# Optimization experiments

Measured on AMD Instinct MI355X. Metric: run time of the kernel, lower is better.

Reference implementation:

```python
import jax, jax.numpy as jnp
import numpy as np

TAU = 10.0 / 7.0
V_TH = 1.0
ALPHA = 10.0  # sigmoid surrogate slope

@jax.custom_vjp
def spike_fn(v):
    # Heaviside(v - v_th) forward, sigmoid surrogate backward
    return (v >= V_TH).astype(v.dtype)

def _spike_fwd(v):
    return spike_fn(v), v

def _spike_bwd(v, g):
    s = jax.nn.sigmoid(ALPHA * (v - V_TH))
    return (g * ALPHA * s * (1.0 - s),)

spike_fn.defvjp(_spike_fwd, _spike_bwd)

def lif_multistep(x_bctm):
    # x: [B, C, T, M]; LIF recurrence over T axis, v_reset=0 hard reset,
    # decay_input=True: v = v + (x - v)/tau
    x_t = jnp.moveaxis(x_bctm, 2, 0)  # [T, B, C, M]
    def step(v, x):
        v = v + (x - v) / TAU
        s = spike_fn(v)
        v = v * (1.0 - s)  # hard reset to 0 (not detached)
        return v, s
    v0 = jnp.zeros_like(x_t[0])
    _, s_t = jax.lax.scan(step, v0, x_t)
    return jnp.moveaxis(s_t, 0, 2)  # [B, C, T, M]

def conv2d(x, w, pad, dil):
    return jax.lax.conv_general_dilated(
        x, w, window_strides=(1, 1),
        padding=[(pad[0], pad[0]), (pad[1], pad[1])],
        rhs_dilation=dil,
        dimension_numbers=('NCHW', 'OIHW', 'NCHW'))

def setup_inputs() -> dict:
    key = jax.random.key(0)
    k0, k1, k2, k3, k4 = jax.random.split(key, 5)
    B, T, M = 32, 128, 40
    x = jax.random.normal(k0, (B, 1, T, M), dtype=jnp.float32)
    # kaiming-ish init: std = 1/sqrt(fan_in)
    w1 = jax.random.normal(k1, (64, 1, 4, 3), dtype=jnp.float32) / np.sqrt(1 * 4 * 3)
    w2 = jax.random.normal(k2, (64, 64, 4, 3), dtype=jnp.float32) / np.sqrt(64 * 4 * 3)
    w3 = jax.random.normal(k3, (64, 64, 4, 3), dtype=jnp.float32) / np.sqrt(64 * 4 * 3)
    kw, kb = jax.random.split(k4)
    wf = jax.random.normal(kw, (12, 64 * 40), dtype=jnp.float32) / np.sqrt(64 * 40)
    bf = jnp.zeros((12,), dtype=jnp.float32)
    return {"x": x, "w1": w1, "w2": w2, "w3": w3, "wf": wf, "bf": bf}

def reference(x, w1, w2, w3, wf, bf):
    h = conv2d(x, w1, (2, 1), (1, 1))     # [B,64,T+1,40]
    h = lif_multistep(h)
    h = conv2d(h, w2, (6, 3), (4, 3))     # shape preserved
    h = lif_multistep(h)
    h = conv2d(h, w3, (24, 9), (16, 9))   # shape preserved
    h = lif_multistep(h)
    B, C, T, M = h.shape
    h = jnp.transpose(h, (0, 2, 1, 3)).reshape(B, T, C * M)  # flatten=True path
    y = h @ wf.T + bf                     # [B, T, 12]
    return y.mean(axis=1)                 # [B, 12]
```

## Files before the change

kernel.cpp:

```cpp
#include <hip/hip_runtime.h>


typedef __attribute__((ext_vector_type(8))) _Float16 v8h;
typedef __attribute__((ext_vector_type(16))) float v16f;
typedef _Float16 half_t;

#define NB 32
#define NC 64
#define NT 129
#define TIN 128
#define NM 40
#define MS8 80
#define ROWB8 3280
#define SROWB8 2560

__global__ void prep_wfrag(const float* __restrict__ w, uint4* __restrict__ wf) {
    int tid = blockIdx.x * 256 + threadIdx.x;
    if (tid >= 12288) return;
    int lane = tid & 63;
    int rest = tid >> 6;
    int hl = rest & 1;
    int ct = (rest >> 1) & 1;
    int cq = (rest >> 2) & 3;
    int tap = rest >> 4;
    int kh = tap / 3, kw = tap % 3;
    int co = ct * 32 + (lane & 31);
    unsigned short o[8];
#pragma unroll
    for (int jj = 0; jj < 8; jj++) {
        int ci = cq * 16 + (lane >> 5) * 8 + jj;
        float wv = w[((co * 64 + ci) * 4 + kh) * 3 + kw];
        _Float16 hi = (_Float16)wv;
        _Float16 val = hl ? (_Float16)((wv - (float)hi) * 2048.0f) : hi;
        unsigned short us;
        __builtin_memcpy(&us, &val, 2);
        o[jj] = us;
    }
    uint4 r;
    __builtin_memcpy(&r, o, 16);
    wf[tid] = r;
}

__global__ void conv1_lif1(const float* __restrict__ x, const float* __restrict__ w1,
                           unsigned char* __restrict__ s1) {
    const int mg = blockIdx.x;
    const int b = blockIdx.y;
    const int c = threadIdx.x & 63;
    const int ml = threadIdx.x >> 6;
    const int m = mg * 4 + ml;
    float w[4][3];
#pragma unroll
    for (int kh = 0; kh < 4; kh++)
#pragma unroll
        for (int kw = 0; kw < 3; kw++) w[kh][kw] = w1[(c * 4 + kh) * 3 + kw];
    const float* xb = x + (size_t)b * TIN * NM;

    float xw[12][3];
#pragma unroll
    for (int rr = 0; rr < 12; rr++)
#pragma unroll
        for (int kw = 0; kw < 3; kw++) xw[rr][kw] = 0.f;
#pragma unroll
    for (int rr = 2; rr < 4; rr++)
#pragma unroll
        for (int kw = 0; kw < 3; kw++) {
            int mc = m - 1 + kw;
            xw[rr][kw] = ((unsigned)mc < (unsigned)NM) ? xb[(rr - 2) * NM + mc] : 0.f;
        }

    unsigned char* orow = s1 + ((size_t)b * NT * NM + m) * 64 + c;
    float v = 0.f;
    const float TAUc = 10.0f / 7.0f;

    for (int tb = 0; tb < NT; tb += 8) {
#pragma unroll
        for (int q = 0; q < 8; q++) {
            int row = tb + 2 + q;
#pragma unroll
            for (int kw = 0; kw < 3; kw++) {
                int mc = m - 1 + kw;
                xw[4 + q][kw] = (row < TIN && (unsigned)mc < (unsigned)NM)
                                    ? xb[row * NM + mc] : 0.f;
            }
        }
        int kmax = (NT - tb) < 8 ? (NT - tb) : 8;
#pragma unroll
        for (int k = 0; k < 8; k++) {
            if (k < kmax) {
                float uacc = 0.f;
#pragma unroll
                for (int kh = 0; kh < 4; kh++)
#pragma unroll
                    for (int kw = 0; kw < 3; kw++) uacc += xw[k + kh][kw] * w[kh][kw];
                v = v + (uacc - v) / TAUc;
                orow[(size_t)(tb + k) * NM * 64] = (v >= 1.0f) ? 1 : 0;
                if (v >= 1.0f) v = 0.0f;
            }
        }
#pragma unroll
        for (int rr = 0; rr < 4; rr++)
#pragma unroll
            for (int kw = 0; kw < 3; kw++) xw[rr][kw] = xw[8 + rr][kw];
    }
}

__device__ inline v8h expand01(uint2 raw) {
    unsigned o0 = __builtin_amdgcn_perm(0u, raw.x, 0x04010400u) * 0x3C00u;
    unsigned o1 = __builtin_amdgcn_perm(0u, raw.x, 0x04030402u) * 0x3C00u;
    unsigned o2 = __builtin_amdgcn_perm(0u, raw.y, 0x04010400u) * 0x3C00u;
    unsigned o3 = __builtin_amdgcn_perm(0u, raw.y, 0x04030402u) * 0x3C00u;
    uint4 o = make_uint4(o0, o1, o2, o3);
    return __builtin_bit_cast(v8h, o);
}

template <int DH, int PH, int DW, int PW, int RMOD>
__global__ __launch_bounds__(256, 3) void convW(const unsigned char* __restrict__ spk,
                                                const uint4* __restrict__ wfrag,
                                                float* __restrict__ u) {
    __shared__ uint4 ldsq[7 * ROWB8 / 16];
    char* lds = (char*)ldsq;
    const int tid = threadIdx.x;
    const int lane = tid & 63;
    const int wv = tid >> 6;
    const int wp = wv >> 1;
    const int hl = wv & 1;
    const int bx = blockIdx.x;
    const int b = blockIdx.y;
    int r, jj0;
    if (bx < 32) { r = bx % RMOD; jj0 = (bx / RMOD) * 4; }
    else         { r = 0;         jj0 = (32 / RMOD) * 4; }

    const char* spb = (const char*)spk + (size_t)b * NT * SROWB8;
#pragma unroll
    for (int k = 0; k < 5; k++) {
        int c = tid + k * 256;
        if (c < 1148) {
            int i = c / 164;
            int rem = c - i * 164;
            int s = rem >> 2;
            int q = rem & 3;
            int tg = r - PH + DH * (jj0 + i);
            uint4 val = make_uint4(0u, 0u, 0u, 0u);
            if ((unsigned)tg < (unsigned)NT && s < 40)
                val = *(const uint4*)(spb + ((size_t)tg * NM + s) * 64 + q * 16);
            *(uint4*)(lds + i * ROWB8 + s * MS8 + q * 16) = val;
        }
    }
    __syncthreads();

    const int pos = lane & 31;
    const int jl = pos >> 4;
    const int ml = pos & 15;
    const int hseg = lane >> 5;
    const int jj = jj0 + 2 * wp + jl;
    const int ldsrow = 2 * wp + jl;
    const int t = r + DH * jj;
    const int mtb[3] = {0, 16, 24};

    int P[3][3];
#pragma unroll
    for (int mt = 0; mt < 3; mt++)
#pragma unroll
        for (int kw = 0; kw < 3; kw++) {
            int md = mtb[mt] + ml + kw * DW - PW;
            int sel = ((unsigned)md < 40u) ? md : 40;
            P[mt][kw] = ldsrow * ROWB8 + sel * MS8 + hseg * 8;
        }

    v16f acc[3][2];
#pragma unroll
    for (int a = 0; a < 3; a++)
#pragma unroll
        for (int c2 = 0; c2 < 2; c2++) acc[a][c2] = (v16f)(0.0f);

    const int hl64 = hl * 64;
#pragma unroll
    for (int tap = 0; tap < 12; tap++) {
        const int kh = tap / 3, kw = tap % 3;
#pragma unroll
        for (int cq = 0; cq < 4; cq++) {
            const uint4* wq = wfrag + (tap * 4 + cq) * 256 + hl64 + lane;
            uint4 a0 = wq[0];
            uint4 a1 = wq[128];
            uint2 r0 = *(const uint2*)(lds + P[0][kw] + kh * ROWB8 + cq * 16);
            uint2 r1 = *(const uint2*)(lds + P[1][kw] + kh * ROWB8 + cq * 16);
            uint2 r2 = *(const uint2*)(lds + P[2][kw] + kh * ROWB8 + cq * 16);
            v8h B0 = expand01(r0);
            v8h B1 = expand01(r1);
            v8h B2 = expand01(r2);
            v8h A0 = __builtin_bit_cast(v8h, a0);
            v8h A1 = __builtin_bit_cast(v8h, a1);
            acc[0][0] = __builtin_amdgcn_mfma_f32_32x32x16_f16(A0, B0, acc[0][0], 0, 0, 0);
            acc[0][1] = __builtin_amdgcn_mfma_f32_32x32x16_f16(A1, B0, acc[0][1], 0, 0, 0);
            acc[1][0] = __builtin_amdgcn_mfma_f32_32x32x16_f16(A0, B1, acc[1][0], 0, 0, 0);
            acc[1][1] = __builtin_amdgcn_mfma_f32_32x32x16_f16(A1, B1, acc[1][1], 0, 0, 0);
            acc[2][0] = __builtin_amdgcn_mfma_f32_32x32x16_f16(A0, B2, acc[2][0], 0, 0, 0);
            acc[2][1] = __builtin_amdgcn_mfma_f32_32x32x16_f16(A1, B2, acc[2][1], 0, 0, 0);
        }
    }

    const float invs = 1.0f / 2048.0f;
    float4* lred = (float4*)lds;
    __syncthreads();
#pragma unroll
    for (int mt = 0; mt < 3; mt++) {
        if (hl) {
#pragma unroll
            for (int ct = 0; ct < 2; ct++)
#pragma unroll
                for (int g = 0; g < 4; g++) {
                    float4 vv;
                    vv.x = acc[mt][ct][4 * g + 0];
                    vv.y = acc[mt][ct][4 * g + 1];
                    vv.z = acc[mt][ct][4 * g + 2];
                    vv.w = acc[mt][ct][4 * g + 3];
                    lred[(wp * 8 + ct * 4 + g) * 64 + lane] = vv;
                }
        }
        __syncthreads();
        if (!hl && t < NT) {
            int m = mtb[mt] + ml;
            float* base = u + ((size_t)(b * NT + t) * NM + m) * 64;
#pragma unroll
            for (int ct = 0; ct < 2; ct++)
#pragma unroll
                for (int g = 0; g < 4; g++) {
                    float4 lo = lred[(wp * 8 + ct * 4 + g) * 64 + lane];
                    int co = ct * 32 + 8 * g + 4 * hseg;
                    float4 val;
                    val.x = acc[mt][ct][4 * g + 0] + lo.x * invs;
                    val.y = acc[mt][ct][4 * g + 1] + lo.y * invs;
                    val.z = acc[mt][ct][4 * g + 2] + lo.z * invs;
                    val.w = acc[mt][ct][4 * g + 3] + lo.w * invs;
                    *(float4*)(base + co) = val;
                }
        }
        __syncthreads();
    }
}

__global__ void lif_spikes(const float* __restrict__ u, unsigned char* __restrict__ s2) {
    int tid = blockIdx.x * 256 + threadIdx.x;
    int b = tid / 2560;
    int cm = tid % 2560;
    const float* up = u + (size_t)b * NT * 2560 + cm;
    unsigned char* sp = s2 + (size_t)b * NT * 2560 + cm;
    float v = 0.f;
    const float TAUc = 10.0f / 7.0f;
    for (int tb = 0; tb < 128; tb += 16) {
        float uu[16];
#pragma unroll
        for (int k = 0; k < 16; k++) uu[k] = up[(size_t)(tb + k) * 2560];
#pragma unroll
        for (int k = 0; k < 16; k++) {
            v = v + (uu[k] - v) / TAUc;
            sp[(size_t)(tb + k) * 2560] = (v >= 1.0f) ? 1 : 0;
            if (v >= 1.0f) v = 0.f;
        }
    }
    float uu = up[(size_t)128 * 2560];
    v = v + (uu - v) / TAUc;
    sp[(size_t)128 * 2560] = (v >= 1.0f) ? 1 : 0;
}

__global__ void lif_sum(const float* __restrict__ u, float* __restrict__ hsum) {
    int tid = blockIdx.x * 256 + threadIdx.x;
    int b = tid / 2560;
    int cm = tid % 2560;
    int m = cm >> 6;
    int co = cm & 63;
    const float* up = u + (size_t)b * NT * 2560 + cm;
    float v = 0.f, cnt = 0.f;
    const float TAUc = 10.0f / 7.0f;
    for (int tb = 0; tb < 128; tb += 16) {
        float uu[16];
#pragma unroll
        for (int k = 0; k < 16; k++) uu[k] = up[(size_t)(tb + k) * 2560];
#pragma unroll
        for (int k = 0; k < 16; k++) {
            v = v + (uu[k] - v) / TAUc;
            if (v >= 1.0f) { cnt += 1.0f; v = 0.f; }
        }
    }
    float uu = up[(size_t)128 * 2560];
    v = v + (uu - v) / TAUc;
    if (v >= 1.0f) cnt += 1.0f;
    hsum[b * 2560 + co * NM + m] = cnt;
}

__global__ void fc_out(const float* __restrict__ hsum, const float* __restrict__ wf,
                       const float* __restrict__ bfv, float* __restrict__ out) {
    int b = blockIdx.x;
    int tid = threadIdx.x;
    float p[12];
#pragma unroll
    for (int k = 0; k < 12; k++) p[k] = 0.0f;
    for (int cm = tid; cm < NC * NM; cm += 256) {
        float h = hsum[b * NC * NM + cm];
#pragma unroll
        for (int k = 0; k < 12; k++) p[k] += h * wf[k * (NC * NM) + cm];
    }
    __shared__ float red[12][4];
    int lane = tid & 63, w = tid >> 6;
#pragma unroll
    for (int k = 0; k < 12; k++) {
        float s = p[k];
#pragma unroll
        for (int off = 32; off > 0; off >>= 1) s += __shfl_down(s, off, 64);
        if (lane == 0) red[k][w] = s;
    }
    __syncthreads();
    if (tid < 12) {
        float s = red[tid][0] + red[tid][1] + red[tid][2] + red[tid][3];
        out[b * 12 + tid] = bfv[tid] + s / 129.0f;
    }
}

extern "C" void kernel_launch(void* const* d_in, const int* in_sizes, int n_in,
                              void* d_out, int out_size, void* d_ws, size_t ws_size,
                              hipStream_t stream) {
    const float* x  = (const float*)d_in[0];
    const float* w1 = (const float*)d_in[1];
    const float* w2 = (const float*)d_in[2];
    const float* w3 = (const float*)d_in[3];
    const float* wf = (const float*)d_in[4];
    const float* bf = (const float*)d_in[5];
    float* out = (float*)d_out;

    char* ws = (char*)d_ws;
    unsigned char* s1 = (unsigned char*)ws;
    unsigned char* s2 = (unsigned char*)(ws + 10567680);
    float*  u   = (float*)(ws + 21135360);
    uint4*  wf2 = (uint4*)(ws + 63406080);
    uint4*  wf3 = (uint4*)(ws + 63602688);
    float* hsum = (float*)(ws + 63799296);

    prep_wfrag<<<48, 256, 0, stream>>>(w2, wf2);
    prep_wfrag<<<48, 256, 0, stream>>>(w3, wf3);

    conv1_lif1<<<dim3(10, 32), 256, 0, stream>>>(x, w1, s1);

    convW<4, 6, 3, 3, 4><<<dim3(33, 32), 256, 0, stream>>>(s1, wf2, u);
    lif_spikes<<<320, 256, 0, stream>>>(u, s2);

    convW<16, 24, 9, 9, 16><<<dim3(33, 32), 256, 0, stream>>>(s2, wf3, u);
    lif_sum<<<320, 256, 0, stream>>>(u, hsum);

    fc_out<<<32, 256, 0, stream>>>(hsum, wf, bf, out);
}
```

Baseline: 218.9 us.

## Prefetch next tap's weight fragments and shrink LDS row stride in convW

New measurement: 224.3 us. 1.02x slower.

```diff
diff --git a/kernel.cpp b/kernel.cpp
--- a/kernel.cpp
+++ b/kernel.cpp
@@ -10,8 +10,8 @@
 #define NT 129
 #define TIN 128
 #define NM 40
-#define MS8 80
-#define ROWB8 3280
+#define MS8 72
+#define ROWB8 2952
 #define SROWB8 2560
 
 __global__ void prep_wfrag(const float* __restrict__ w, uint4* __restrict__ wf) {
@@ -114,10 +114,10 @@
 }
 
 template <int DH, int PH, int DW, int PW, int RMOD>
-__global__ __launch_bounds__(256, 3) void convW(const unsigned char* __restrict__ spk,
+__global__ __launch_bounds__(256, 2) void convW(const unsigned char* __restrict__ spk,
                                                 const uint4* __restrict__ wfrag,
                                                 float* __restrict__ u) {
-    __shared__ uint4 ldsq[7 * ROWB8 / 16];
+    __shared__ uint2 ldsq[7 * ROWB8 / 8];
     char* lds = (char*)ldsq;
     const int tid = threadIdx.x;
     const int lane = tid & 63;
@@ -132,18 +132,18 @@
 
     const char* spb = (const char*)spk + (size_t)b * NT * SROWB8;
 #pragma unroll
-    for (int k = 0; k < 5; k++) {
+    for (int k = 0; k < 9; k++) {
         int c = tid + k * 256;
-        if (c < 1148) {
-            int i = c / 164;
-            int rem = c - i * 164;
-            int s = rem >> 2;
-            int q = rem & 3;
+        if (c < 2296) {
+            int i = c / 328;
+            int rem = c - i * 328;
+            int s = rem >> 3;
+            int q = rem & 7;
             int tg = r - PH + DH * (jj0 + i);
-            uint4 val = make_uint4(0u, 0u, 0u, 0u);
+            uint2 val = make_uint2(0u, 0u);
             if ((unsigned)tg < (unsigned)NT && s < 40)
-                val = *(const uint4*)(spb + ((size_t)tg * NM + s) * 64 + q * 16);
-            *(uint4*)(lds + i * ROWB8 + s * MS8 + q * 16) = val;
+                val = *(const uint2*)(spb + ((size_t)tg * NM + s) * 64 + q * 8);
+            *(uint2*)(lds + i * ROWB8 + s * MS8 + q * 8) = val;
         }
     }
     __syncthreads();
@@ -174,28 +174,48 @@
         for (int c2 = 0; c2 < 2; c2++) acc[a][c2] = (v16f)(0.0f);
 
     const int hl64 = hl * 64;
+    uint4 cA0[4], cA1[4], nA0[4], nA1[4];
+#pragma unroll
+    for (int cq = 0; cq < 4; cq++) {
+        const uint4* wq = wfrag + cq * 256 + hl64 + lane;
+        cA0[cq] = wq[0];
+        cA1[cq] = wq[128];
+    }
+
 #pragma unroll
     for (int tap = 0; tap < 12; tap++) {
+        if (tap < 11) {
+#pragma unroll
+            for (int cq = 0; cq < 4; cq++) {
+                const uint4* wq = wfrag + ((tap + 1) * 4 + cq) * 256 + hl64 + lane;
+                nA0[cq] = wq[0];
+                nA1[cq] = wq[128];
+            }
+        }
         const int kh = tap / 3, kw = tap % 3;
 #pragma unroll
         for (int cq = 0; cq < 4; cq++) {
-            const uint4* wq = wfrag + (tap * 4 + cq) * 256 + hl64 + lane;
-            uint4 a0 = wq[0];
-            uint4 a1 = wq[128];
             uint2 r0 = *(const uint2*)(lds + P[0][kw] + kh * ROWB8 + cq * 16);
             uint2 r1 = *(const uint2*)(lds + P[1][kw] + kh * ROWB8 + cq * 16);
             uint2 r2 = *(const uint2*)(lds + P[2][kw] + kh * ROWB8 + cq * 16);
             v8h B0 = expand01(r0);
             v8h B1 = expand01(r1);
             v8h B2 = expand01(r2);
-            v8h A0 = __builtin_bit_cast(v8h, a0);
-            v8h A1 = __builtin_bit_cast(v8h, a1);
+            v8h A0 = __builtin_bit_cast(v8h, cA0[cq]);
+            v8h A1 = __builtin_bit_cast(v8h, cA1[cq]);
             acc[0][0] = __builtin_amdgcn_mfma_f32_32x32x16_f16(A0, B0, acc[0][0], 0, 0, 0);
             acc[0][1] = __builtin_amdgcn_mfma_f32_32x32x16_f16(A1, B0, acc[0][1], 0, 0, 0);
             acc[1][0] = __builtin_amdgcn_mfma_f32_32x32x16_f16(A0, B1, acc[1][0], 0, 0, 0);
             acc[1][1] = __builtin_amdgcn_mfma_f32_32x32x16_f16(A1, B1, acc[1][1], 0, 0, 0);
             acc[2][0] = __builtin_amdgcn_mfma_f32_32x32x16_f16(A0, B2, acc[2][0], 0, 0, 0);
             acc[2][1] = __builtin_amdgcn_mfma_f32_32x32x16_f16(A1, B2, acc[2][1], 0, 0, 0);
+        }
+        if (tap < 11) {
+#pragma unroll
+            for (int cq = 0; cq < 4; cq++) {
+                cA0[cq] = nA0[cq];
+                cA1[cq] = nA1[cq];
+            }
         }
     }
 
```
